# Kernel optimization log

Hardware: AMD Instinct MI355X
Metric: run time of the kernel (lower is better)

Reference implementation:

```python
import jax, jax.numpy as jnp
import numpy as np

TEMPERATURE = 0.5
B, D = 4096, 256

def setup_inputs() -> dict:
    key = jax.random.key(0)
    k1, k2 = jax.random.split(key)
    z_i = jax.random.normal(k1, (B, D), dtype=jnp.float32)
    z_j = jax.random.normal(k2, (B, D), dtype=jnp.float32)
    return {"z_i": z_i, "z_j": z_j}

def reference(z_i, z_j):
    # NT-Xent loss (SimCLR). Cosine similarity of L2-normalized rows == dot product.
    b = z_i.shape[0]
    n = 2 * b
    zi = z_i / jnp.linalg.norm(z_i, axis=1, keepdims=True)
    zj = z_j / jnp.linalg.norm(z_j, axis=1, keepdims=True)
    z = jnp.concatenate([zi, zj], axis=0)            # [N, D]
    sim = jnp.matmul(z, z.T)                          # [N, N] cosine-sim matrix
    # positives: sim(i, i+b) and sim(i+b, i)
    pos = jnp.concatenate([jnp.diagonal(sim, offset=b), jnp.diagonal(sim, offset=-b)])  # [N]
    logits = sim / TEMPERATURE
    # Cross-entropy with the positive as the target class over {pos} U negatives.
    # The candidate set per row is all j != i (the positive j = partner(i) is included,
    # only the self-similarity diagonal is excluded) -> mask diagonal with -inf.
    neg_inf = jnp.asarray(-jnp.inf, dtype=logits.dtype)
    masked = jnp.where(jnp.eye(n, dtype=bool), neg_inf, logits)
    lse = jax.nn.logsumexp(masked, axis=1)            # [N]
    loss = jnp.sum(lse - pos / TEMPERATURE) / n
    return loss
```

## Files before the change

kernel.cpp:

```cpp
#include <hip/hip_runtime.h>
#include <hip/hip_bf16.h>


constexpr int BB = 4096;
constexpr int NN = 8192;
constexpr int DD = 256;
constexpr int RT = 256;
constexpr int CC = 512;
constexpr int NRT = NN / RT;
constexpr int NCH = NN / CC;
constexpr int CSTEPS = CC / 32;

typedef _Float16 half4v __attribute__((ext_vector_type(4)));
typedef _Float16 half8v __attribute__((ext_vector_type(8)));
typedef float floatx16 __attribute__((ext_vector_type(16)));

__global__ __launch_bounds__(256) void nt_normalize(
    const float* __restrict__ zi, const float* __restrict__ zj,
    _Float16* __restrict__ Z, float* __restrict__ posPartial,
    float* __restrict__ rowsum)
{
    const int lane = threadIdx.x & 63;
    const int wave = threadIdx.x >> 6;
    const int i = blockIdx.x * 4 + wave;

    if (blockIdx.x < 32) rowsum[blockIdx.x * 256 + threadIdx.x] = 0.f;

    const float4 a = ((const float4*)(zi + (size_t)i * DD))[lane];
    const float4 b = ((const float4*)(zj + (size_t)i * DD))[lane];

    float ssi = a.x*a.x + a.y*a.y + a.z*a.z + a.w*a.w;
    float ssj = b.x*b.x + b.y*b.y + b.z*b.z + b.w*b.w;
    float dd  = a.x*b.x + a.y*b.y + a.z*b.z + a.w*b.w;
#pragma unroll
    for (int off = 32; off > 0; off >>= 1) {
        ssi += __shfl_xor(ssi, off);
        ssj += __shfl_xor(ssj, off);
        dd  += __shfl_xor(dd,  off);
    }
    const float invi = rsqrtf(ssi);
    const float invj = rsqrtf(ssj);

    half4v ha, hb;
    ha.x = (_Float16)(a.x * invi); ha.y = (_Float16)(a.y * invi);
    ha.z = (_Float16)(a.z * invi); ha.w = (_Float16)(a.w * invi);
    hb.x = (_Float16)(b.x * invj); hb.y = (_Float16)(b.y * invj);
    hb.z = (_Float16)(b.z * invj); hb.w = (_Float16)(b.w * invj);

    ((half4v*)(Z + (size_t)i * DD))[lane]        = ha;
    ((half4v*)(Z + (size_t)(BB + i) * DD))[lane] = hb;

    __shared__ float ps[4];
    if (lane == 0) ps[wave] = dd * invi * invj;
    __syncthreads();
    if (threadIdx.x == 0)
        posPartial[blockIdx.x] = ps[0] + ps[1] + ps[2] + ps[3];
}

__global__ __launch_bounds__(256, 2) void nt_simexp(
    const _Float16* __restrict__ Z, float* __restrict__ rowsum)
{
    __shared__ _Float16 lds[32 * DD];

    const int bid = blockIdx.x;
    const int rt = bid & (NRT - 1);
    const int ch = bid >> 5;
    const int tid = threadIdx.x;
    const int wave = tid >> 6;
    const int lane = tid & 63;
    const int lm = lane & 31;
    const int lh = lane >> 5;

    const int rbase = rt * RT + wave * 64;

    half8v bfrag[2][16];
#pragma unroll
    for (int b = 0; b < 2; ++b) {
        const _Float16* rowp = Z + (size_t)(rbase + b * 32 + lm) * DD + lh * 8;
#pragma unroll
        for (int s = 0; s < 16; ++s)
            bfrag[b][s] = *(const half8v*)(rowp + s * 16);
    }

    const int g_c0 = tid >> 5;
    const int g_kc = tid & 31;

    half8v pre[4];
    auto loadTile = [&](int cbase) {
#pragma unroll
        for (int it = 0; it < 4; ++it) {
            const int c = g_c0 + it * 8;
            pre[it] = *(const half8v*)(Z + (size_t)(cbase + c) * DD + g_kc * 8);
        }
    };
    auto storeTile = [&]() {
#pragma unroll
        for (int it = 0; it < 4; ++it) {
            const int c = g_c0 + it * 8;
            *(half8v*)(&lds[c * DD + (g_kc ^ (c & 7)) * 8]) = pre[it];
        }
    };

    float ea0 = 0.f, ea1 = 0.f;
    const int cchunk = ch * CC;
    const bool blockdiag = (ch == (rt >> 1));
    const float KEXP = 2.0f * 1.44269504088896340736f;

    loadTile(cchunk);
    storeTile();

    for (int cs = 0; cs < CSTEPS; ++cs) {
        const int cbase = cchunk + cs * 32;

        __syncthreads();
        if (cs + 1 < CSTEPS) loadTile(cchunk + (cs + 1) * 32);

        floatx16 c0, c1;
#pragma unroll
        for (int r = 0; r < 16; ++r) { c0[r] = 0.f; c1[r] = 0.f; }

#pragma unroll
        for (int s = 0; s < 16; ++s) {
            const int phys = (2 * s + lh) ^ (lm & 7);
            half8v af = *(const half8v*)(&lds[lm * DD + phys * 8]);
            c0 = __builtin_amdgcn_mfma_f32_32x32x16_f16(af, bfrag[0][s], c0, 0, 0, 0);
            c1 = __builtin_amdgcn_mfma_f32_32x32x16_f16(af, bfrag[1][s], c1, 0, 0, 0);
        }

        const bool m0 = blockdiag && (cbase == rbase);
        const bool m1 = blockdiag && (cbase == rbase + 32);
        if (!(m0 | m1)) {
#pragma unroll
            for (int r = 0; r < 16; ++r) {
                ea0 += __builtin_amdgcn_exp2f(c0[r] * KEXP);
                ea1 += __builtin_amdgcn_exp2f(c1[r] * KEXP);
            }
        } else {
#pragma unroll
            for (int r = 0; r < 16; ++r) {
                const int mrow = (r & 3) + 8 * (r >> 2) + 4 * lh;
                float e0 = __builtin_amdgcn_exp2f(c0[r] * KEXP);
                float e1 = __builtin_amdgcn_exp2f(c1[r] * KEXP);
                if (m0 && (mrow == lm)) e0 = 0.f;
                if (m1 && (mrow == lm)) e1 = 0.f;
                ea0 += e0; ea1 += e1;
            }
        }

        __syncthreads();
        if (cs + 1 < CSTEPS) storeTile();
    }

    ea0 += __shfl_xor(ea0, 32);
    ea1 += __shfl_xor(ea1, 32);
    if (lane < 32) {
        atomicAdd(&rowsum[rbase + lm], ea0);
        atomicAdd(&rowsum[rbase + 32 + lm], ea1);
    }
}

__global__ __launch_bounds__(256) void nt_finalize(
    const float* __restrict__ rowsum, const float* __restrict__ posPartial,
    float* __restrict__ out)
{
    const int tid = threadIdx.x;
    float acc = 0.f;
#pragma unroll
    for (int it = 0; it < NN / 256; ++it)
        acc += __builtin_amdgcn_logf(rowsum[tid + it * 256]);
    float pacc = 0.f;
#pragma unroll
    for (int it = 0; it < 4; ++it)
        pacc += posPartial[tid + it * 256];

#pragma unroll
    for (int off = 32; off > 0; off >>= 1) {
        acc  += __shfl_xor(acc,  off);
        pacc += __shfl_xor(pacc, off);
    }
    __shared__ float sa[4], sp[4];
    const int wave = tid >> 6;
    if ((tid & 63) == 0) { sa[wave] = acc; sp[wave] = pacc; }
    __syncthreads();
    if (tid == 0) {
        const float lntot = (sa[0] + sa[1] + sa[2] + sa[3]) * 0.6931471805599453f;
        const float ptot  = sp[0] + sp[1] + sp[2] + sp[3];
        out[0] = (lntot - 4.0f * ptot) * (1.0f / (float)NN);
    }
}

extern "C" void kernel_launch(void* const* d_in, const int* in_sizes, int n_in,
                              void* d_out, int out_size, void* d_ws, size_t ws_size,
                              hipStream_t stream) {
    const float* zi = (const float*)d_in[0];
    const float* zj = (const float*)d_in[1];
    float* out = (float*)d_out;

    _Float16* Z = (_Float16*)d_ws;
    float* rowsum = (float*)((char*)d_ws + (size_t)NN * DD * 2);
    float* posPartial = rowsum + NN;

    nt_normalize<<<BB / 4, 256, 0, stream>>>(zi, zj, Z, posPartial, rowsum);
    nt_simexp<<<NRT * NCH, 256, 0, stream>>>((const _Float16*)Z, rowsum);
    nt_finalize<<<1, 256, 0, stream>>>(rowsum, posPartial, out);
}
```

Baseline: 98.23 us.

## Exploit similarity matrix symmetry: compute upper-triangle tiles and accumulate column sums

```diff
diff --git a/kernel.cpp b/kernel.cpp
--- a/kernel.cpp
+++ b/kernel.cpp
@@ -5,11 +5,10 @@
 constexpr int BB = 4096;
 constexpr int NN = 8192;
 constexpr int DD = 256;
-constexpr int RT = 256;
-constexpr int CC = 512;
-constexpr int NRT = NN / RT;
-constexpr int NCH = NN / CC;
-constexpr int CSTEPS = CC / 32;
+constexpr int TILE = 256;
+constexpr int NT = NN / TILE;
+constexpr int NBLK = NT * (NT + 1) / 2;
+constexpr int CSTEPS = TILE / 32;
 
 typedef _Float16 half4v __attribute__((ext_vector_type(4)));
 typedef _Float16 half8v __attribute__((ext_vector_type(8)));
@@ -57,21 +56,44 @@
         posPartial[blockIdx.x] = ps[0] + ps[1] + ps[2] + ps[3];
 }
 
+__device__ __forceinline__ float half_sums(float x) {
+    int t;
+    t = __builtin_amdgcn_update_dpp(0, __builtin_bit_cast(int, x), 0x111, 0xf, 0xf, false);
+    x += __builtin_bit_cast(float, t);
+    t = __builtin_amdgcn_update_dpp(0, __builtin_bit_cast(int, x), 0x112, 0xf, 0xf, false);
+    x += __builtin_bit_cast(float, t);
+    t = __builtin_amdgcn_update_dpp(0, __builtin_bit_cast(int, x), 0x114, 0xf, 0xf, false);
+    x += __builtin_bit_cast(float, t);
+    t = __builtin_amdgcn_update_dpp(0, __builtin_bit_cast(int, x), 0x118, 0xf, 0xf, false);
+    x += __builtin_bit_cast(float, t);
+    t = __builtin_amdgcn_update_dpp(0, __builtin_bit_cast(int, x), 0x142, 0xa, 0xf, false);
+    x += __builtin_bit_cast(float, t);
+    return x;
+}
+
 __global__ __launch_bounds__(256, 2) void nt_simexp(
     const _Float16* __restrict__ Z, float* __restrict__ rowsum)
 {
-    __shared__ _Float16 lds[32 * DD];
-
-    const int bid = blockIdx.x;
-    const int rt = bid & (NRT - 1);
-    const int ch = bid >> 5;
+    __shared__ _Float16 lds[2][32 * DD];
+    __shared__ float colacc[TILE];
+
+    int bid = (blockIdx.x & 7) * (NBLK / 8) + (blockIdx.x >> 3);
+
+    int rt = 0, rem = bid;
+    while (rem >= NT - rt) { rem -= NT - rt; ++rt; }
+    const int ct = rt + rem;
+    const bool diag = (rt == ct);
+
     const int tid = threadIdx.x;
     const int wave = tid >> 6;
     const int lane = tid & 63;
     const int lm = lane & 31;
     const int lh = lane >> 5;
 
-    const int rbase = rt * RT + wave * 64;
+    const int rbase = rt * TILE + wave * 64;
+    const int cbase0 = ct * TILE;
+
+    colacc[tid] = 0.f;
 
     half8v bfrag[2][16];
 #pragma unroll
@@ -86,35 +108,32 @@
     const int g_kc = tid & 31;
 
     half8v pre[4];
-    auto loadTile = [&](int cbase) {
+    auto loadTile = [&](int crow0) {
 #pragma unroll
         for (int it = 0; it < 4; ++it) {
             const int c = g_c0 + it * 8;
-            pre[it] = *(const half8v*)(Z + (size_t)(cbase + c) * DD + g_kc * 8);
+            pre[it] = *(const half8v*)(Z + (size_t)(crow0 + c) * DD + g_kc * 8);
         }
     };
-    auto storeTile = [&]() {
+    auto storeTile = [&](int bi) {
 #pragma unroll
         for (int it = 0; it < 4; ++it) {
             const int c = g_c0 + it * 8;
-            *(half8v*)(&lds[c * DD + (g_kc ^ (c & 7)) * 8]) = pre[it];
+            *(half8v*)(&lds[bi][c * DD + (g_kc ^ (c & 7)) * 8]) = pre[it];
         }
     };
 
     float ea0 = 0.f, ea1 = 0.f;
-    const int cchunk = ch * CC;
-    const bool blockdiag = (ch == (rt >> 1));
     const float KEXP = 2.0f * 1.44269504088896340736f;
 
-    loadTile(cchunk);
-    storeTile();
+    loadTile(cbase0);
+    storeTile(0);
 
     for (int cs = 0; cs < CSTEPS; ++cs) {
-        const int cbase = cchunk + cs * 32;
-
         __syncthreads();
-        if (cs + 1 < CSTEPS) loadTile(cchunk + (cs + 1) * 32);
-
+        if (cs + 1 < CSTEPS) loadTile(cbase0 + (cs + 1) * 32);
+
+        const _Float16* buf = lds[cs & 1];
         floatx16 c0, c1;
 #pragma unroll
         for (int r = 0; r < 16; ++r) { c0[r] = 0.f; c1[r] = 0.f; }
@@ -122,20 +141,26 @@
 #pragma unroll
         for (int s = 0; s < 16; ++s) {
             const int phys = (2 * s + lh) ^ (lm & 7);
-            half8v af = *(const half8v*)(&lds[lm * DD + phys * 8]);
+            half8v af = *(const half8v*)(&buf[lm * DD + phys * 8]);
             c0 = __builtin_amdgcn_mfma_f32_32x32x16_f16(af, bfrag[0][s], c0, 0, 0, 0);
             c1 = __builtin_amdgcn_mfma_f32_32x32x16_f16(af, bfrag[1][s], c1, 0, 0, 0);
         }
 
-        const bool m0 = blockdiag && (cbase == rbase);
-        const bool m1 = blockdiag && (cbase == rbase + 32);
-        if (!(m0 | m1)) {
+        if (!diag) {
 #pragma unroll
             for (int r = 0; r < 16; ++r) {
-                ea0 += __builtin_amdgcn_exp2f(c0[r] * KEXP);
-                ea1 += __builtin_amdgcn_exp2f(c1[r] * KEXP);
+                float e0 = __builtin_amdgcn_exp2f(c0[r] * KEXP);
+                float e1 = __builtin_amdgcn_exp2f(c1[r] * KEXP);
+                ea0 += e0; ea1 += e1;
+                float s2 = half_sums(e0 + e1);
+                if (lm == 31) {
+                    const int cidx = cs * 32 + (r & 3) + 8 * (r >> 2) + 4 * lh;
+                    atomicAdd(&colacc[cidx], s2);
+                }
             }
         } else {
+            const bool m0 = (cs == 2 * wave);
+            const bool m1 = (cs == 2 * wave + 1);
 #pragma unroll
             for (int r = 0; r < 16; ++r) {
                 const int mrow = (r & 3) + 8 * (r >> 2) + 4 * lh;
@@ -147,8 +172,7 @@
             }
         }
 
-        __syncthreads();
-        if (cs + 1 < CSTEPS) storeTile();
+        if (cs + 1 < CSTEPS) storeTile((cs + 1) & 1);
     }
 
     ea0 += __shfl_xor(ea0, 32);
@@ -156,6 +180,11 @@
     if (lane < 32) {
         atomicAdd(&rowsum[rbase + lm], ea0);
         atomicAdd(&rowsum[rbase + 32 + lm], ea1);
+    }
+
+    if (!diag) {
+        __syncthreads();
+        atomicAdd(&rowsum[cbase0 + tid], colacc[tid]);
     }
 }
 
@@ -201,6 +230,6 @@
     float* posPartial = rowsum + NN;
 
     nt_normalize<<<BB / 4, 256, 0, stream>>>(zi, zj, Z, posPartial, rowsum);
-    nt_simexp<<<NRT * NCH, 256, 0, stream>>>((const _Float16*)Z, rowsum);
+    nt_simexp<<<NBLK, 256, 0, stream>>>((const _Float16*)Z, rowsum);
     nt_finalize<<<1, 256, 0, stream>>>(rowsum, posPartial, out);
 }
```

Measured after the change: 99.89 us. About the same (+1.7%).
